# Performance work log

Measured on AMD Instinct MI355X. Metric: run time of the kernel, lower is better.

Reference implementation:

```python
import jax, jax.numpy as jnp
import numpy as np

B, N, D, K = 2, 8192, 512, 16


def setup_inputs() -> dict:
    key = jax.random.key(0)
    k1, k2, k3, k4 = jax.random.split(key, 4)
    x = jax.random.normal(k1, (B, N, D), dtype=jnp.float32)
    xyz = jax.random.normal(k2, (B, N, 3), dtype=jnp.float32)
    # nn.Linear(d_model, 3*d_model): weight [3D, D], bias [3D]
    W_qkv = jax.random.normal(k3, (3 * D, D), dtype=jnp.float32) * 0.02
    b_qkv = jnp.zeros((3 * D,), dtype=jnp.float32)
    # nn.Linear(d_model, d_model)
    W_fc = jax.random.normal(k4, (D, D), dtype=jnp.float32) * 0.02
    b_fc = jnp.zeros((D,), dtype=jnp.float32)
    return {"x": x, "xyz": xyz, "W_qkv": W_qkv, "b_qkv": b_qkv, "W_fc": W_fc, "b_fc": b_fc}


def _knn_idx(xyz):
    # squared-distance KNN (same ordering as cdist): |a|^2 + |b|^2 - 2 a.b
    sq = jnp.sum(xyz * xyz, axis=-1)                      # [B, N]
    d2 = sq[:, :, None] + sq[:, None, :] - 2.0 * jnp.einsum('bnc,bmc->bnm', xyz, xyz)
    return jax.lax.top_k(-d2, K)[1]                       # [B, N, K] smallest distances


def reference(x, xyz, W_qkv, b_qkv, W_fc, b_fc):
    knn_idx = _knn_idx(xyz)                               # no-grad in original
    qkv = jnp.einsum('bnd,ed->bne', x, W_qkv) + b_qkv     # [B, N, 3D]
    qkv = qkv.reshape(B, N, 3, D)
    q, k, v = qkv[:, :, 0], qkv[:, :, 1], qkv[:, :, 2]    # [B, N, D]
    gather = jax.vmap(lambda arr, idx: arr[idx])          # per-batch neighbor gather
    k_neigh = gather(k, knn_idx)                          # [B, N, K, D]
    v_neigh = gather(v, knn_idx)                          # [B, N, K, D]
    # faithful to einsum('bnd,bnsk->bns', q, k_neigh): sums d and feature dims independently
    attn = (q.sum(-1)[:, :, None] * k_neigh.sum(-1)) / jnp.sqrt(jnp.float32(D))  # [B, N, K]
    attn = jax.nn.softmax(attn, axis=2)[..., None]        # [B, N, K, 1]
    x_out = (attn * v_neigh).sum(axis=2)                  # [B, N, D]
    return jnp.einsum('bnd,ed->bne', x_out, W_fc) + b_fc + x
```

## Files before the change

### kernel.cpp

```cpp
#include <hip/hip_runtime.h>

typedef _Float16 half_t;
typedef _Float16 half8 __attribute__((ext_vector_type(8)));
typedef _Float16 half4v __attribute__((ext_vector_type(4)));
typedef float f32x4 __attribute__((ext_vector_type(4)));
typedef float f32x2 __attribute__((ext_vector_type(2)));

#define NB 2
#define NN 8192
#define ND 512
#define NKNN 16
#define BN (NB*NN)

#define OFF_XH   0ull
#define OFF_VH   (OFF_XH  + (size_t)BN*ND*2)
#define OFF_XOH  (OFF_VH  + (size_t)BN*ND*2)
#define OFF_WVH  (OFF_XOH + (size_t)BN*ND*2)
#define OFF_WFCH (OFF_WVH + (size_t)ND*ND*2)
#define OFF_XW   (OFF_WFCH+ (size_t)ND*ND*2)
#define OFF_XW2  (OFF_XW  + (size_t)BN*16)
#define OFF_IDX  (OFF_XW2 + (size_t)BN*16)
#define OFF_WQC  (OFF_IDX + (size_t)BN*NKNN*4)
#define OFF_WKC  (OFF_WQC + 2048)
#define OFF_QKB  (OFF_WKC + 2048)
#define OFF_QS   (OFF_QKB + 256)
#define OFF_KS   (OFF_QS  + (size_t)BN*4)

__global__ __launch_bounds__(256) void kcolsum(const float* __restrict__ W,
                                               float* __restrict__ wq,
                                               float* __restrict__ wk) {
  int h = blockIdx.x >> 3, g = blockIdx.x & 7;
  int t = threadIdx.x, dl = t & 63, s = t >> 6;
  const float* Wb = W + (size_t)h * 512 * 512;
  int d = g * 64 + dl;
  float acc = 0.f;
  for (int e = s * 128; e < s * 128 + 128; ++e) acc += Wb[(size_t)e * 512 + d];
  __shared__ float red[4][64];
  red[s][dl] = acc;
  __syncthreads();
  if (s == 0) (h ? wk : wq)[d] = red[0][dl] + red[1][dl] + red[2][dl] + red[3][dl];
}

__global__ __launch_bounds__(512) void kbias(const float* __restrict__ b,
                                             float* __restrict__ qkb) {
  __shared__ float r0[512], r1[512];
  int t = threadIdx.x;
  r0[t] = b[t]; r1[t] = b[512 + t];
  __syncthreads();
  for (int s = 256; s; s >>= 1) {
    if (t < s) { r0[t] += r0[t + s]; r1[t] += r1[t + s]; }
    __syncthreads();
  }
  if (t == 0) { qkb[0] = r0[0]; qkb[1] = r1[0]; }
}

__global__ __launch_bounds__(256) void kconvw(const float* __restrict__ wqkv,
                                              const float* __restrict__ wfc,
                                              half_t* __restrict__ wvh,
                                              half_t* __restrict__ wfch) {
  int i = blockIdx.x * 256 + threadIdx.x;
  float4 a = ((const float4*)(wqkv + 1024 * 512))[i];
  half4v ha; ha[0]=(half_t)a.x; ha[1]=(half_t)a.y; ha[2]=(half_t)a.z; ha[3]=(half_t)a.w;
  *(half4v*)(wvh + (size_t)i * 4) = ha;
  float4 c = ((const float4*)wfc)[i];
  half4v hc; hc[0]=(half_t)c.x; hc[1]=(half_t)c.y; hc[2]=(half_t)c.z; hc[3]=(half_t)c.w;
  *(half4v*)(wfch + (size_t)i * 4) = hc;
}

__global__ __launch_bounds__(256) void kxh(const float* __restrict__ x,
                                           const float* __restrict__ wq,
                                           const float* __restrict__ wk,
                                           const float* __restrict__ qkb,
                                           half_t* __restrict__ xh,
                                           float* __restrict__ qs,
                                           float* __restrict__ ks) {
  int wid = blockIdx.x * 4 + (threadIdx.x >> 6);
  int l = threadIdx.x & 63;
  size_t base = (size_t)wid * ND + l * 8;
  float4 a0 = *(const float4*)(x + base);
  float4 a1 = *(const float4*)(x + base + 4);
  half8 h;
  h[0]=(half_t)a0.x; h[1]=(half_t)a0.y; h[2]=(half_t)a0.z; h[3]=(half_t)a0.w;
  h[4]=(half_t)a1.x; h[5]=(half_t)a1.y; h[6]=(half_t)a1.z; h[7]=(half_t)a1.w;
  *(half8*)(xh + base) = h;
  float4 q0 = ((const float4*)(wq + l * 8))[0], q1 = ((const float4*)(wq + l * 8))[1];
  float4 k0 = ((const float4*)(wk + l * 8))[0], k1 = ((const float4*)(wk + l * 8))[1];
  float dq = a0.x*q0.x + a0.y*q0.y + a0.z*q0.z + a0.w*q0.w
           + a1.x*q1.x + a1.y*q1.y + a1.z*q1.z + a1.w*q1.w;
  float dk = a0.x*k0.x + a0.y*k0.y + a0.z*k0.z + a0.w*k0.w
           + a1.x*k1.x + a1.y*k1.y + a1.z*k1.z + a1.w*k1.w;
  #pragma unroll
  for (int o = 32; o; o >>= 1) { dq += __shfl_xor(dq, o); dk += __shfl_xor(dk, o); }
  if (l == 0) { qs[wid] = dq + qkb[0]; ks[wid] = dk + qkb[1]; }
}

__global__ __launch_bounds__(256) void kxyzw(const float* __restrict__ xyz,
                                             float4* __restrict__ xw,
                                             float4* __restrict__ xw2) {
  int p = blockIdx.x * 256 + threadIdx.x;
  int b = p >> 12;
  int pl = p & 4095;
  int i0 = b * NN + pl * 2;
  const float* s = xyz + (size_t)i0 * 3;
  float x0 = s[0], y0 = s[1], z0 = s[2];
  float x1 = s[3], y1 = s[4], z1 = s[5];
  float sq0 = __fadd_rn(__fadd_rn(__fmul_rn(x0, x0), __fmul_rn(y0, y0)), __fmul_rn(z0, z0));
  float sq1 = __fadd_rn(__fadd_rn(__fmul_rn(x1, x1), __fmul_rn(y1, y1)), __fmul_rn(z1, z1));
  xw[i0]     = make_float4(x0, y0, z0, sq0);
  xw[i0 + 1] = make_float4(x1, y1, z1, sq1);
  xw2[(size_t)b * NN + pl]          = make_float4(x0, x1, y0, y1);
  xw2[(size_t)b * NN + NN/2 + pl]   = make_float4(z0, z1, sq0, sq1);
}

#define QPW 4
__global__ __launch_bounds__(256, 4) void kknn(const float4* __restrict__ xw,
                                               const float4* __restrict__ xw2,
                                               int* __restrict__ idxo) {
  const int tid = threadIdx.x;
  const int l = tid & 63;
  const int b = blockIdx.x >> 9;
  const int qbase = (blockIdx.x & 511) * (4 * QPW) + (tid >> 6) * QPW;
  const float4* xb  = xw  + (size_t)b * NN;
  const float4* xa2 = xw2 + (size_t)b * NN;
  const float4* xb2 = xa2 + NN / 2;

  f32x2 qxx[QPW], qyy[QPW], qzz[QPW], qww[QPW];
  #pragma unroll
  for (int qi = 0; qi < QPW; ++qi) {
    float4 qp = xb[qbase + qi];
    qxx[qi] = (f32x2){qp.x, qp.x};
    qyy[qi] = (f32x2){qp.y, qp.y};
    qzz[qi] = (f32x2){qp.z, qp.z};
    qww[qi] = (f32x2){qp.w, qp.w};
  }
  const f32x2 m2 = (f32x2){-2.0f, -2.0f};

  float mind0[QPW], mind1[QPW]; int mini0[QPW], mini1[QPW];
  #pragma unroll
  for (int qi = 0; qi < QPW; ++qi) {
    mind0[qi] = __builtin_inff(); mini0[qi] = 0x7fffffff;
    mind1[qi] = __builtin_inff(); mini1[qi] = 0x7fffffff;
  }

  auto body1 = [&](const float4& A, const float4& Bv, int it) {
    f32x2 cx = (f32x2){A.x, A.y};
    f32x2 cy = (f32x2){A.z, A.w};
    f32x2 cz = (f32x2){Bv.x, Bv.y};
    f32x2 cw = (f32x2){Bv.z, Bv.w};
    int ci0 = (it * 64 + l) * 2;
    #pragma unroll
    for (int qi = 0; qi < QPW; ++qi) {
      f32x2 dot = __builtin_elementwise_fma(qzz[qi], cz,
                    __builtin_elementwise_fma(qyy[qi], cy, qxx[qi] * cx));
      f32x2 s2 = qww[qi] + cw;
      f32x2 d2 = __builtin_elementwise_fma(m2, dot, s2);
      if (d2.x < mind0[qi]) { mind0[qi] = d2.x; mini0[qi] = ci0; }
      if (d2.y < mind1[qi]) { mind1[qi] = d2.y; mini1[qi] = ci0 + 1; }
    }
  };

  {
    float4 A0 = xa2[l],      B0 = xb2[l];
    float4 A1 = xa2[64 + l], B1 = xb2[64 + l];
    for (int tt = 0; tt < 4; ++tt) {
      __syncthreads();
      #pragma unroll
      for (int its = 0; its < 16; its += 2) {
        int it = tt * 16 + its;
        int pf = it + 2; if (pf > 62) pf = 62;
        float4 A2 = xa2[pf * 64 + l];
        float4 B2 = xb2[pf * 64 + l];
        float4 A3 = xa2[pf * 64 + 64 + l];
        float4 B3 = xb2[pf * 64 + 64 + l];
        body1(A0, B0, it);
        body1(A1, B1, it + 1);
        A0 = A2; B0 = B2; A1 = A3; B1 = B3;
      }
    }
  }

  float mind[QPW]; int mini[QPW];
  #pragma unroll
  for (int qi = 0; qi < QPW; ++qi) {
    bool take1 = (mind1[qi] < mind0[qi]) ||
                 (mind1[qi] == mind0[qi] && mini1[qi] < mini0[qi]);
    mind[qi] = take1 ? mind1[qi] : mind0[qi];
    mini[qi] = take1 ? mini1[qi] : mini0[qi];
  }

  float kd[QPW]; int ki[QPW]; float wst[QPW];
  #pragma unroll
  for (int qi = 0; qi < QPW; ++qi) {
    float d = mind[qi]; int ii = mini[qi];
    #pragma unroll
    for (int k = 2; k <= 64; k <<= 1) {
      #pragma unroll
      for (int j = k >> 1; j > 0; j >>= 1) {
        float od = __shfl_xor(d, j);
        int   oi = __shfl_xor(ii, j);
        bool up = ((l & k) == 0);
        bool lower_lane = ((l & j) == 0);
        bool oless = (od < d) || (od == d && oi < ii);
        bool take = (up == lower_lane) ? oless : !oless;
        if (take) { d = od; ii = oi; }
      }
    }
    kd[qi] = __shfl(d, l & 15);
    ki[qi] = __shfl(ii, l & 15);
    wst[qi] = __shfl(d, 15);
  }

  auto insert = [&](bool ok, float dv, int iv, int qi) {
    unsigned long long m = __ballot(ok);
    while (m) {
      int a = __builtin_ctzll(m);
      m &= m - 1;
      float dc = __shfl(dv, a);
      int ic = __shfl(iv, a);
      bool lower = (kd[qi] < dc) || (kd[qi] == dc && ki[qi] < ic);
      int r = __popcll(__ballot(lower) & 0xFFFFull);
      if (r < 16) {
        float pd = __shfl_up(kd[qi], 1, 16);
        int pi = __shfl_up(ki[qi], 1, 16);
        int pp = l & 15;
        if (pp == r)      { kd[qi] = dc; ki[qi] = ic; }
        else if (pp > r)  { kd[qi] = pd; ki[qi] = pi; }
        wst[qi] = __shfl(kd[qi], 15, 16);
      }
    }
  };

  auto body2 = [&](const float4& A, const float4& Bv, int it) {
    f32x2 cx = (f32x2){A.x, A.y};
    f32x2 cy = (f32x2){A.z, A.w};
    f32x2 cz = (f32x2){Bv.x, Bv.y};
    f32x2 cw = (f32x2){Bv.z, Bv.w};
    int ci0 = (it * 64 + l) * 2;
    #pragma unroll
    for (int qi = 0; qi < QPW; ++qi) {
      f32x2 dot = __builtin_elementwise_fma(qzz[qi], cz,
                    __builtin_elementwise_fma(qyy[qi], cy, qxx[qi] * cx));
      f32x2 s2 = qww[qi] + cw;
      f32x2 d2 = __builtin_elementwise_fma(m2, dot, s2);
      bool ok0 = (d2.x <= wst[qi]) && (ci0 != mini[qi]);
      bool ok1 = (d2.y <= wst[qi]) && (ci0 + 1 != mini[qi]);
      insert(ok0, d2.x, ci0, qi);
      insert(ok1, d2.y, ci0 + 1, qi);
    }
  };

  {
    float4 A0 = xa2[l],      B0 = xb2[l];
    float4 A1 = xa2[64 + l], B1 = xb2[64 + l];
    for (int tt = 0; tt < 4; ++tt) {
      __syncthreads();
      #pragma unroll
      for (int its = 0; its < 16; its += 2) {
        int it = tt * 16 + its;
        int pf = it + 2; if (pf > 62) pf = 62;
        float4 A2 = xa2[pf * 64 + l];
        float4 B2 = xb2[pf * 64 + l];
        float4 A3 = xa2[pf * 64 + 64 + l];
        float4 B3 = xb2[pf * 64 + 64 + l];
        body2(A0, B0, it);
        body2(A1, B1, it + 1);
        A0 = A2; B0 = B2; A1 = A3; B1 = B3;
      }
    }
  }

  if (l < 16) {
    #pragma unroll
    for (int qi = 0; qi < QPW; ++qi)
      idxo[((size_t)b * NN + qbase + qi) * NKNN + l] = ki[qi];
  }
}

__device__ __forceinline__ void gload16(const void* g, void* l) {
  __builtin_amdgcn_global_load_lds((const __attribute__((address_space(1))) void*)g,
                                   (__attribute__((address_space(3))) void*)l, 16, 0, 0);
}

template <int EPI>
__global__ __launch_bounds__(256) void kgemm(const half_t* __restrict__ A,
                                             const half_t* __restrict__ Bw,
                                             const float* __restrict__ bias,
                                             const float* __restrict__ resid,
                                             void* __restrict__ Cout) {
  __shared__ __align__(16) half_t As[128 * 64];
  __shared__ __align__(16) half_t Bs[128 * 64];
  const int tid = threadIdx.x;
  const int l = tid & 63;
  const int w = tid >> 6;
  const int wm = w >> 1, wn = w & 1;
  const int mt = blockIdx.x >> 2;
  const int nt = blockIdx.x & 3;
  const int lr = l & 15, lg = l >> 4;

  f32x4 acc[4][4];
  #pragma unroll
  for (int i = 0; i < 4; ++i)
    #pragma unroll
    for (int j = 0; j < 4; ++j) acc[i][j] = (f32x4){0.f, 0.f, 0.f, 0.f};

  for (int kt = 0; kt < 8; ++kt) {
    #pragma unroll
    for (int i = 0; i < 4; ++i) {
      int id = i * 256 + tid;
      int rr = id >> 3, cc = id & 7;
      gload16(A + (size_t)(mt * 128 + rr) * ND + kt * 64 + cc * 8,
              (void*)(As + (size_t)(i * 256 + w * 64) * 8));
      gload16(Bw + (size_t)(nt * 128 + rr) * ND + kt * 64 + cc * 8,
              (void*)(Bs + (size_t)(i * 256 + w * 64) * 8));
    }
    __syncthreads();
    #pragma unroll
    for (int kk = 0; kk < 2; ++kk) {
      half8 af[4], bf[4];
      #pragma unroll
      for (int mi = 0; mi < 4; ++mi)
        af[mi] = *(const half8*)(As + (wm * 64 + mi * 16 + lr) * 64 + kk * 32 + lg * 8);
      #pragma unroll
      for (int ni = 0; ni < 4; ++ni)
        bf[ni] = *(const half8*)(Bs + (wn * 64 + ni * 16 + lr) * 64 + kk * 32 + lg * 8);
      #pragma unroll
      for (int mi = 0; mi < 4; ++mi)
        #pragma unroll
        for (int ni = 0; ni < 4; ++ni)
          acc[mi][ni] = __builtin_amdgcn_mfma_f32_16x16x32_f16(af[mi], bf[ni], acc[mi][ni], 0, 0, 0);
    }
    __syncthreads();
  }

  #pragma unroll
  for (int mi = 0; mi < 4; ++mi) {
    #pragma unroll
    for (int ni = 0; ni < 4; ++ni) {
      int col = nt * 128 + wn * 64 + ni * 16 + lr;
      #pragma unroll
      for (int r4 = 0; r4 < 4; ++r4) {
        size_t row = (size_t)mt * 128 + wm * 64 + mi * 16 + lg * 4 + r4;
        float v = acc[mi][ni][r4] + bias[col];
        if (EPI == 0) ((half_t*)Cout)[row * ND + col] = (half_t)v;
        else          ((float*)Cout)[row * ND + col] = v + resid[row * ND + col];
      }
    }
  }
}

__global__ __launch_bounds__(256) void kattn(const int* __restrict__ idx,
                                             const float* __restrict__ qs,
                                             const float* __restrict__ ks,
                                             const half_t* __restrict__ vh,
                                             half_t* __restrict__ xoh) {
  int wid = blockIdx.x * 4 + (threadIdx.x >> 6);
  int l = threadIdx.x & 63;
  int b = wid >> 13;
  int j = l & 15;
  int nb = idx[(size_t)wid * NKNN + j];
  float ksv = ks[(size_t)b * NN + nb];
  float logit = __fdiv_rn(__fmul_rn(qs[wid], ksv), 22.627416997969522f);
  float mx = logit;
  #pragma unroll
  for (int o = 8; o; o >>= 1) mx = fmaxf(mx, __shfl_xor(mx, o, 16));
  float e = expf(logit - mx);
  float s = e;
  #pragma unroll
  for (int o = 8; o; o >>= 1) s += __shfl_xor(s, o, 16);
  float p = e / s;

  float acc[8] = {0.f, 0.f, 0.f, 0.f, 0.f, 0.f, 0.f, 0.f};
  #pragma unroll
  for (int t16 = 0; t16 < 16; ++t16) {
    float wj = __shfl(p, t16, 16);
    int ij = __shfl(nb, t16, 16);
    const half8 vv = *(const half8*)(vh + ((size_t)b * NN + ij) * ND + l * 8);
    #pragma unroll
    for (int u = 0; u < 8; ++u) acc[u] += wj * (float)vv[u];
  }
  half8 ho;
  #pragma unroll
  for (int u = 0; u < 8; ++u) ho[u] = (half_t)acc[u];
  *(half8*)(xoh + (size_t)wid * ND + l * 8) = ho;
}

extern "C" void kernel_launch(void* const* d_in, const int* in_sizes, int n_in,
                              void* d_out, int out_size, void* d_ws, size_t ws_size,
                              hipStream_t stream) {
  const float* x    = (const float*)d_in[0];
  const float* xyz  = (const float*)d_in[1];
  const float* wqkv = (const float*)d_in[2];
  const float* bqkv = (const float*)d_in[3];
  const float* wfc  = (const float*)d_in[4];
  const float* bfc  = (const float*)d_in[5];
  char* ws = (char*)d_ws;
  half_t* xh   = (half_t*)(ws + OFF_XH);
  half_t* vh   = (half_t*)(ws + OFF_VH);
  half_t* xoh  = (half_t*)(ws + OFF_XOH);
  half_t* wvh  = (half_t*)(ws + OFF_WVH);
  half_t* wfch = (half_t*)(ws + OFF_WFCH);
  float4* xw   = (float4*)(ws + OFF_XW);
  float4* xw2  = (float4*)(ws + OFF_XW2);
  int*    idx  = (int*)(ws + OFF_IDX);
  float*  wqc  = (float*)(ws + OFF_WQC);
  float*  wkc  = (float*)(ws + OFF_WKC);
  float*  qkb  = (float*)(ws + OFF_QKB);
  float*  qs   = (float*)(ws + OFF_QS);
  float*  ks   = (float*)(ws + OFF_KS);

  kcolsum<<<dim3(16),  dim3(256), 0, stream>>>(wqkv, wqc, wkc);
  kbias  <<<dim3(1),   dim3(512), 0, stream>>>(bqkv, qkb);
  kconvw <<<dim3(256), dim3(256), 0, stream>>>(wqkv, wfc, wvh, wfch);
  kxyzw  <<<dim3(32),  dim3(256), 0, stream>>>(xyz, xw, xw2);
  kxh    <<<dim3(4096),dim3(256), 0, stream>>>(x, wqc, wkc, qkb, xh, qs, ks);
  kknn   <<<dim3(1024),dim3(256), 0, stream>>>(xw, xw2, idx);
  kgemm<0><<<dim3(512),dim3(256), 0, stream>>>(xh, wvh, bqkv + 1024, (const float*)nullptr, (void*)vh);
  kattn  <<<dim3(4096),dim3(256), 0, stream>>>(idx, qs, ks, vh, xoh);
  kgemm<1><<<dim3(512),dim3(256), 0, stream>>>(xoh, wfch, bfc, x, d_out);
}
```

Baseline: 167.2 us.

## Merge setup kernels and co-schedule KNN, q/k sums and V GEMM in one launch

Four small setup kernels are folded into one block-indexed launch. KNN, the q/k row-sum computation and the V projection GEMM now run as role-partitioned blocks of a single grid, so their independent work can overlap on the GPU. The fp16 copy of x is dropped: the GEMM blocks read fp32 x and convert it to half in registers before writing LDS, which removes one global round trip. The risk is that the heterogeneous blocks compete for occupancy, since the KNN launch bound now also applies to the GEMM blocks. The GEMM's A-side load also changes from the asynchronous global-to-LDS path to synchronous register loads.

```diff
diff --git a/kernel.cpp b/kernel.cpp
--- a/kernel.cpp
+++ b/kernel.cpp
@@ -26,323 +26,322 @@
 #define OFF_QS   (OFF_QKB + 256)
 #define OFF_KS   (OFF_QS  + (size_t)BN*4)
 
-__global__ __launch_bounds__(256) void kcolsum(const float* __restrict__ W,
-                                               float* __restrict__ wq,
-                                               float* __restrict__ wk) {
-  int h = blockIdx.x >> 3, g = blockIdx.x & 7;
-  int t = threadIdx.x, dl = t & 63, s = t >> 6;
-  const float* Wb = W + (size_t)h * 512 * 512;
-  int d = g * 64 + dl;
-  float acc = 0.f;
-  for (int e = s * 128; e < s * 128 + 128; ++e) acc += Wb[(size_t)e * 512 + d];
-  __shared__ float red[4][64];
-  red[s][dl] = acc;
-  __syncthreads();
-  if (s == 0) (h ? wk : wq)[d] = red[0][dl] + red[1][dl] + red[2][dl] + red[3][dl];
-}
-
-__global__ __launch_bounds__(512) void kbias(const float* __restrict__ b,
-                                             float* __restrict__ qkb) {
-  __shared__ float r0[512], r1[512];
-  int t = threadIdx.x;
-  r0[t] = b[t]; r1[t] = b[512 + t];
-  __syncthreads();
-  for (int s = 256; s; s >>= 1) {
-    if (t < s) { r0[t] += r0[t + s]; r1[t] += r1[t + s]; }
-    __syncthreads();
-  }
-  if (t == 0) { qkb[0] = r0[0]; qkb[1] = r1[0]; }
-}
-
-__global__ __launch_bounds__(256) void kconvw(const float* __restrict__ wqkv,
-                                              const float* __restrict__ wfc,
-                                              half_t* __restrict__ wvh,
-                                              half_t* __restrict__ wfch) {
-  int i = blockIdx.x * 256 + threadIdx.x;
-  float4 a = ((const float4*)(wqkv + 1024 * 512))[i];
-  half4v ha; ha[0]=(half_t)a.x; ha[1]=(half_t)a.y; ha[2]=(half_t)a.z; ha[3]=(half_t)a.w;
-  *(half4v*)(wvh + (size_t)i * 4) = ha;
-  float4 c = ((const float4*)wfc)[i];
-  half4v hc; hc[0]=(half_t)c.x; hc[1]=(half_t)c.y; hc[2]=(half_t)c.z; hc[3]=(half_t)c.w;
-  *(half4v*)(wfch + (size_t)i * 4) = hc;
-}
-
-__global__ __launch_bounds__(256) void kxh(const float* __restrict__ x,
-                                           const float* __restrict__ wq,
-                                           const float* __restrict__ wk,
-                                           const float* __restrict__ qkb,
-                                           half_t* __restrict__ xh,
-                                           float* __restrict__ qs,
-                                           float* __restrict__ ks) {
-  int wid = blockIdx.x * 4 + (threadIdx.x >> 6);
-  int l = threadIdx.x & 63;
-  size_t base = (size_t)wid * ND + l * 8;
-  float4 a0 = *(const float4*)(x + base);
-  float4 a1 = *(const float4*)(x + base + 4);
-  half8 h;
-  h[0]=(half_t)a0.x; h[1]=(half_t)a0.y; h[2]=(half_t)a0.z; h[3]=(half_t)a0.w;
-  h[4]=(half_t)a1.x; h[5]=(half_t)a1.y; h[6]=(half_t)a1.z; h[7]=(half_t)a1.w;
-  *(half8*)(xh + base) = h;
-  float4 q0 = ((const float4*)(wq + l * 8))[0], q1 = ((const float4*)(wq + l * 8))[1];
-  float4 k0 = ((const float4*)(wk + l * 8))[0], k1 = ((const float4*)(wk + l * 8))[1];
-  float dq = a0.x*q0.x + a0.y*q0.y + a0.z*q0.z + a0.w*q0.w
-           + a1.x*q1.x + a1.y*q1.y + a1.z*q1.z + a1.w*q1.w;
-  float dk = a0.x*k0.x + a0.y*k0.y + a0.z*k0.z + a0.w*k0.w
-           + a1.x*k1.x + a1.y*k1.y + a1.z*k1.z + a1.w*k1.w;
-  #pragma unroll
-  for (int o = 32; o; o >>= 1) { dq += __shfl_xor(dq, o); dk += __shfl_xor(dk, o); }
-  if (l == 0) { qs[wid] = dq + qkb[0]; ks[wid] = dk + qkb[1]; }
-}
-
-__global__ __launch_bounds__(256) void kxyzw(const float* __restrict__ xyz,
-                                             float4* __restrict__ xw,
-                                             float4* __restrict__ xw2) {
-  int p = blockIdx.x * 256 + threadIdx.x;
-  int b = p >> 12;
-  int pl = p & 4095;
-  int i0 = b * NN + pl * 2;
-  const float* s = xyz + (size_t)i0 * 3;
-  float x0 = s[0], y0 = s[1], z0 = s[2];
-  float x1 = s[3], y1 = s[4], z1 = s[5];
-  float sq0 = __fadd_rn(__fadd_rn(__fmul_rn(x0, x0), __fmul_rn(y0, y0)), __fmul_rn(z0, z0));
-  float sq1 = __fadd_rn(__fadd_rn(__fmul_rn(x1, x1), __fmul_rn(y1, y1)), __fmul_rn(z1, z1));
-  xw[i0]     = make_float4(x0, y0, z0, sq0);
-  xw[i0 + 1] = make_float4(x1, y1, z1, sq1);
-  xw2[(size_t)b * NN + pl]          = make_float4(x0, x1, y0, y1);
-  xw2[(size_t)b * NN + NN/2 + pl]   = make_float4(z0, z1, sq0, sq1);
-}
-
-#define QPW 4
-__global__ __launch_bounds__(256, 4) void kknn(const float4* __restrict__ xw,
-                                               const float4* __restrict__ xw2,
-                                               int* __restrict__ idxo) {
-  const int tid = threadIdx.x;
-  const int l = tid & 63;
-  const int b = blockIdx.x >> 9;
-  const int qbase = (blockIdx.x & 511) * (4 * QPW) + (tid >> 6) * QPW;
-  const float4* xb  = xw  + (size_t)b * NN;
-  const float4* xa2 = xw2 + (size_t)b * NN;
-  const float4* xb2 = xa2 + NN / 2;
-
-  f32x2 qxx[QPW], qyy[QPW], qzz[QPW], qww[QPW];
-  #pragma unroll
-  for (int qi = 0; qi < QPW; ++qi) {
-    float4 qp = xb[qbase + qi];
-    qxx[qi] = (f32x2){qp.x, qp.x};
-    qyy[qi] = (f32x2){qp.y, qp.y};
-    qzz[qi] = (f32x2){qp.z, qp.z};
-    qww[qi] = (f32x2){qp.w, qp.w};
-  }
-  const f32x2 m2 = (f32x2){-2.0f, -2.0f};
-
-  float mind0[QPW], mind1[QPW]; int mini0[QPW], mini1[QPW];
-  #pragma unroll
-  for (int qi = 0; qi < QPW; ++qi) {
-    mind0[qi] = __builtin_inff(); mini0[qi] = 0x7fffffff;
-    mind1[qi] = __builtin_inff(); mini1[qi] = 0x7fffffff;
-  }
-
-  auto body1 = [&](const float4& A, const float4& Bv, int it) {
-    f32x2 cx = (f32x2){A.x, A.y};
-    f32x2 cy = (f32x2){A.z, A.w};
-    f32x2 cz = (f32x2){Bv.x, Bv.y};
-    f32x2 cw = (f32x2){Bv.z, Bv.w};
-    int ci0 = (it * 64 + l) * 2;
-    #pragma unroll
-    for (int qi = 0; qi < QPW; ++qi) {
-      f32x2 dot = __builtin_elementwise_fma(qzz[qi], cz,
-                    __builtin_elementwise_fma(qyy[qi], cy, qxx[qi] * cx));
-      f32x2 s2 = qww[qi] + cw;
-      f32x2 d2 = __builtin_elementwise_fma(m2, dot, s2);
-      if (d2.x < mind0[qi]) { mind0[qi] = d2.x; mini0[qi] = ci0; }
-      if (d2.y < mind1[qi]) { mind1[qi] = d2.y; mini1[qi] = ci0 + 1; }
-    }
-  };
-
-  {
-    float4 A0 = xa2[l],      B0 = xb2[l];
-    float4 A1 = xa2[64 + l], B1 = xb2[64 + l];
-    for (int tt = 0; tt < 4; ++tt) {
-      __syncthreads();
-      #pragma unroll
-      for (int its = 0; its < 16; its += 2) {
-        int it = tt * 16 + its;
-        int pf = it + 2; if (pf > 62) pf = 62;
-        float4 A2 = xa2[pf * 64 + l];
-        float4 B2 = xb2[pf * 64 + l];
-        float4 A3 = xa2[pf * 64 + 64 + l];
-        float4 B3 = xb2[pf * 64 + 64 + l];
-        body1(A0, B0, it);
-        body1(A1, B1, it + 1);
-        A0 = A2; B0 = B2; A1 = A3; B1 = B3;
-      }
-    }
-  }
-
-  float mind[QPW]; int mini[QPW];
-  #pragma unroll
-  for (int qi = 0; qi < QPW; ++qi) {
-    bool take1 = (mind1[qi] < mind0[qi]) ||
-                 (mind1[qi] == mind0[qi] && mini1[qi] < mini0[qi]);
-    mind[qi] = take1 ? mind1[qi] : mind0[qi];
-    mini[qi] = take1 ? mini1[qi] : mini0[qi];
-  }
-
-  float kd[QPW]; int ki[QPW]; float wst[QPW];
-  #pragma unroll
-  for (int qi = 0; qi < QPW; ++qi) {
-    float d = mind[qi]; int ii = mini[qi];
-    #pragma unroll
-    for (int k = 2; k <= 64; k <<= 1) {
-      #pragma unroll
-      for (int j = k >> 1; j > 0; j >>= 1) {
-        float od = __shfl_xor(d, j);
-        int   oi = __shfl_xor(ii, j);
-        bool up = ((l & k) == 0);
-        bool lower_lane = ((l & j) == 0);
-        bool oless = (od < d) || (od == d && oi < ii);
-        bool take = (up == lower_lane) ? oless : !oless;
-        if (take) { d = od; ii = oi; }
-      }
-    }
-    kd[qi] = __shfl(d, l & 15);
-    ki[qi] = __shfl(ii, l & 15);
-    wst[qi] = __shfl(d, 15);
-  }
-
-  auto insert = [&](bool ok, float dv, int iv, int qi) {
-    unsigned long long m = __ballot(ok);
-    while (m) {
-      int a = __builtin_ctzll(m);
-      m &= m - 1;
-      float dc = __shfl(dv, a);
-      int ic = __shfl(iv, a);
-      bool lower = (kd[qi] < dc) || (kd[qi] == dc && ki[qi] < ic);
-      int r = __popcll(__ballot(lower) & 0xFFFFull);
-      if (r < 16) {
-        float pd = __shfl_up(kd[qi], 1, 16);
-        int pi = __shfl_up(ki[qi], 1, 16);
-        int pp = l & 15;
-        if (pp == r)      { kd[qi] = dc; ki[qi] = ic; }
-        else if (pp > r)  { kd[qi] = pd; ki[qi] = pi; }
-        wst[qi] = __shfl(kd[qi], 15, 16);
-      }
-    }
-  };
-
-  auto body2 = [&](const float4& A, const float4& Bv, int it) {
-    f32x2 cx = (f32x2){A.x, A.y};
-    f32x2 cy = (f32x2){A.z, A.w};
-    f32x2 cz = (f32x2){Bv.x, Bv.y};
-    f32x2 cw = (f32x2){Bv.z, Bv.w};
-    int ci0 = (it * 64 + l) * 2;
-    #pragma unroll
-    for (int qi = 0; qi < QPW; ++qi) {
-      f32x2 dot = __builtin_elementwise_fma(qzz[qi], cz,
-                    __builtin_elementwise_fma(qyy[qi], cy, qxx[qi] * cx));
-      f32x2 s2 = qww[qi] + cw;
-      f32x2 d2 = __builtin_elementwise_fma(m2, dot, s2);
-      bool ok0 = (d2.x <= wst[qi]) && (ci0 != mini[qi]);
-      bool ok1 = (d2.y <= wst[qi]) && (ci0 + 1 != mini[qi]);
-      insert(ok0, d2.x, ci0, qi);
-      insert(ok1, d2.y, ci0 + 1, qi);
-    }
-  };
-
-  {
-    float4 A0 = xa2[l],      B0 = xb2[l];
-    float4 A1 = xa2[64 + l], B1 = xb2[64 + l];
-    for (int tt = 0; tt < 4; ++tt) {
-      __syncthreads();
-      #pragma unroll
-      for (int its = 0; its < 16; its += 2) {
-        int it = tt * 16 + its;
-        int pf = it + 2; if (pf > 62) pf = 62;
-        float4 A2 = xa2[pf * 64 + l];
-        float4 B2 = xb2[pf * 64 + l];
-        float4 A3 = xa2[pf * 64 + 64 + l];
-        float4 B3 = xb2[pf * 64 + 64 + l];
-        body2(A0, B0, it);
-        body2(A1, B1, it + 1);
-        A0 = A2; B0 = B2; A1 = A3; B1 = B3;
-      }
-    }
-  }
-
-  if (l < 16) {
-    #pragma unroll
-    for (int qi = 0; qi < QPW; ++qi)
-      idxo[((size_t)b * NN + qbase + qi) * NKNN + l] = ki[qi];
-  }
-}
-
 __device__ __forceinline__ void gload16(const void* g, void* l) {
   __builtin_amdgcn_global_load_lds((const __attribute__((address_space(1))) void*)g,
                                    (__attribute__((address_space(3))) void*)l, 16, 0, 0);
 }
 
-template <int EPI>
-__global__ __launch_bounds__(256) void kgemm(const half_t* __restrict__ A,
-                                             const half_t* __restrict__ Bw,
-                                             const float* __restrict__ bias,
-                                             const float* __restrict__ resid,
-                                             void* __restrict__ Cout) {
-  __shared__ __align__(16) half_t As[128 * 64];
-  __shared__ __align__(16) half_t Bs[128 * 64];
+__global__ __launch_bounds__(256) void ksetup(const float* __restrict__ wqkv,
+                                              const float* __restrict__ bqkv,
+                                              const float* __restrict__ wfc,
+                                              const float* __restrict__ xyz,
+                                              float* __restrict__ wq, float* __restrict__ wk,
+                                              float* __restrict__ qkb,
+                                              half_t* __restrict__ wvh, half_t* __restrict__ wfch,
+                                              float4* __restrict__ xw, float4* __restrict__ xw2) {
+  const int blk = blockIdx.x;
+  const int t = threadIdx.x;
+  if (blk < 16) {
+    int h = blk >> 3, g = blk & 7;
+    int dl = t & 63, s = t >> 6;
+    const float* Wb = wqkv + (size_t)h * 512 * 512;
+    int d = g * 64 + dl;
+    float acc = 0.f;
+    for (int e = s * 128; e < s * 128 + 128; ++e) acc += Wb[(size_t)e * 512 + d];
+    __shared__ float red[4][64];
+    red[s][dl] = acc;
+    __syncthreads();
+    if (s == 0) (h ? wk : wq)[d] = red[0][dl] + red[1][dl] + red[2][dl] + red[3][dl];
+  } else if (blk == 16) {
+    __shared__ float r0[256], r1[256];
+    r0[t] = bqkv[t] + bqkv[t + 256];
+    r1[t] = bqkv[512 + t] + bqkv[768 + t];
+    __syncthreads();
+    for (int s = 128; s; s >>= 1) {
+      if (t < s) { r0[t] += r0[t + s]; r1[t] += r1[t + s]; }
+      __syncthreads();
+    }
+    if (t == 0) { qkb[0] = r0[0]; qkb[1] = r1[0]; }
+  } else if (blk < 273) {
+    int i = (blk - 17) * 256 + t;
+    float4 a = ((const float4*)(wqkv + 1024 * 512))[i];
+    half4v ha; ha[0]=(half_t)a.x; ha[1]=(half_t)a.y; ha[2]=(half_t)a.z; ha[3]=(half_t)a.w;
+    *(half4v*)(wvh + (size_t)i * 4) = ha;
+    float4 c = ((const float4*)wfc)[i];
+    half4v hc; hc[0]=(half_t)c.x; hc[1]=(half_t)c.y; hc[2]=(half_t)c.z; hc[3]=(half_t)c.w;
+    *(half4v*)(wfch + (size_t)i * 4) = hc;
+  } else {
+    int p = (blk - 273) * 256 + t;
+    int b = p >> 12;
+    int pl = p & 4095;
+    int i0 = b * NN + pl * 2;
+    const float* s = xyz + (size_t)i0 * 3;
+    float x0 = s[0], y0 = s[1], z0 = s[2];
+    float x1 = s[3], y1 = s[4], z1 = s[5];
+    float sq0 = __fadd_rn(__fadd_rn(__fmul_rn(x0, x0), __fmul_rn(y0, y0)), __fmul_rn(z0, z0));
+    float sq1 = __fadd_rn(__fadd_rn(__fmul_rn(x1, x1), __fmul_rn(y1, y1)), __fmul_rn(z1, z1));
+    xw[i0]     = make_float4(x0, y0, z0, sq0);
+    xw[i0 + 1] = make_float4(x1, y1, z1, sq1);
+    xw2[(size_t)b * NN + pl]        = make_float4(x0, x1, y0, y1);
+    xw2[(size_t)b * NN + NN/2 + pl] = make_float4(z0, z1, sq0, sq1);
+  }
+}
+
+#define QPW 4
+__global__ __launch_bounds__(256, 4) void kbig(const float4* __restrict__ xw,
+                                               const float4* __restrict__ xw2,
+                                               int* __restrict__ idxo,
+                                               const float* __restrict__ x,
+                                               const float* __restrict__ wq,
+                                               const float* __restrict__ wk,
+                                               const float* __restrict__ qkb,
+                                               float* __restrict__ qs,
+                                               float* __restrict__ ks,
+                                               const half_t* __restrict__ wvh,
+                                               const float* __restrict__ bv,
+                                               half_t* __restrict__ vh) {
+  const int g5 = blockIdx.x / 5;
+  const int r5 = blockIdx.x % 5;
   const int tid = threadIdx.x;
   const int l = tid & 63;
   const int w = tid >> 6;
-  const int wm = w >> 1, wn = w & 1;
-  const int mt = blockIdx.x >> 2;
-  const int nt = blockIdx.x & 3;
-  const int lr = l & 15, lg = l >> 4;
-
-  f32x4 acc[4][4];
-  #pragma unroll
-  for (int i = 0; i < 4; ++i)
-    #pragma unroll
-    for (int j = 0; j < 4; ++j) acc[i][j] = (f32x4){0.f, 0.f, 0.f, 0.f};
-
-  for (int kt = 0; kt < 8; ++kt) {
-    #pragma unroll
-    for (int i = 0; i < 4; ++i) {
-      int id = i * 256 + tid;
-      int rr = id >> 3, cc = id & 7;
-      gload16(A + (size_t)(mt * 128 + rr) * ND + kt * 64 + cc * 8,
-              (void*)(As + (size_t)(i * 256 + w * 64) * 8));
-      gload16(Bw + (size_t)(nt * 128 + rr) * ND + kt * 64 + cc * 8,
-              (void*)(Bs + (size_t)(i * 256 + w * 64) * 8));
-    }
-    __syncthreads();
-    #pragma unroll
-    for (int kk = 0; kk < 2; ++kk) {
-      half8 af[4], bf[4];
-      #pragma unroll
-      for (int mi = 0; mi < 4; ++mi)
-        af[mi] = *(const half8*)(As + (wm * 64 + mi * 16 + lr) * 64 + kk * 32 + lg * 8);
-      #pragma unroll
-      for (int ni = 0; ni < 4; ++ni)
-        bf[ni] = *(const half8*)(Bs + (wn * 64 + ni * 16 + lr) * 64 + kk * 32 + lg * 8);
-      #pragma unroll
-      for (int mi = 0; mi < 4; ++mi)
+
+  if (r5 < 2) {
+    const int bid = g5 * 2 + r5;
+    const int b = bid >> 9;
+    const int qbase = (bid & 511) * (4 * QPW) + w * QPW;
+    const float4* xb  = xw  + (size_t)b * NN;
+    const float4* xa2 = xw2 + (size_t)b * NN;
+    const float4* xb2 = xa2 + NN / 2;
+
+    f32x2 qxx[QPW], qyy[QPW], qzz[QPW], qww[QPW];
+    #pragma unroll
+    for (int qi = 0; qi < QPW; ++qi) {
+      float4 qp = xb[qbase + qi];
+      qxx[qi] = (f32x2){qp.x, qp.x};
+      qyy[qi] = (f32x2){qp.y, qp.y};
+      qzz[qi] = (f32x2){qp.z, qp.z};
+      qww[qi] = (f32x2){qp.w, qp.w};
+    }
+    const f32x2 m2 = (f32x2){-2.0f, -2.0f};
+
+    float mind0[QPW], mind1[QPW]; int mini0[QPW], mini1[QPW];
+    #pragma unroll
+    for (int qi = 0; qi < QPW; ++qi) {
+      mind0[qi] = __builtin_inff(); mini0[qi] = 0x7fffffff;
+      mind1[qi] = __builtin_inff(); mini1[qi] = 0x7fffffff;
+    }
+
+    auto body1 = [&](const float4& A, const float4& Bv, int it) {
+      f32x2 cx = (f32x2){A.x, A.y};
+      f32x2 cy = (f32x2){A.z, A.w};
+      f32x2 cz = (f32x2){Bv.x, Bv.y};
+      f32x2 cw = (f32x2){Bv.z, Bv.w};
+      int ci0 = (it * 64 + l) * 2;
+      #pragma unroll
+      for (int qi = 0; qi < QPW; ++qi) {
+        f32x2 dot = __builtin_elementwise_fma(qzz[qi], cz,
+                      __builtin_elementwise_fma(qyy[qi], cy, qxx[qi] * cx));
+        f32x2 s2 = qww[qi] + cw;
+        f32x2 d2 = __builtin_elementwise_fma(m2, dot, s2);
+        if (d2.x < mind0[qi]) { mind0[qi] = d2.x; mini0[qi] = ci0; }
+        if (d2.y < mind1[qi]) { mind1[qi] = d2.y; mini1[qi] = ci0 + 1; }
+      }
+    };
+
+    {
+      float4 A0 = xa2[l],      B0 = xb2[l];
+      float4 A1 = xa2[64 + l], B1 = xb2[64 + l];
+      for (int tt = 0; tt < 4; ++tt) {
+        __syncthreads();
+        #pragma unroll
+        for (int its = 0; its < 16; its += 2) {
+          int it = tt * 16 + its;
+          int pf = it + 2; if (pf > 62) pf = 62;
+          float4 A2 = xa2[pf * 64 + l];
+          float4 B2 = xb2[pf * 64 + l];
+          float4 A3 = xa2[pf * 64 + 64 + l];
+          float4 B3 = xb2[pf * 64 + 64 + l];
+          body1(A0, B0, it);
+          body1(A1, B1, it + 1);
+          A0 = A2; B0 = B2; A1 = A3; B1 = B3;
+        }
+      }
+    }
+
+    float mind[QPW]; int mini[QPW];
+    #pragma unroll
+    for (int qi = 0; qi < QPW; ++qi) {
+      bool take1 = (mind1[qi] < mind0[qi]) ||
+                   (mind1[qi] == mind0[qi] && mini1[qi] < mini0[qi]);
+      mind[qi] = take1 ? mind1[qi] : mind0[qi];
+      mini[qi] = take1 ? mini1[qi] : mini0[qi];
+    }
+
+    float kd[QPW]; int ki[QPW]; float wst[QPW];
+    #pragma unroll
+    for (int qi = 0; qi < QPW; ++qi) {
+      float d = mind[qi]; int ii = mini[qi];
+      #pragma unroll
+      for (int k = 2; k <= 64; k <<= 1) {
+        #pragma unroll
+        for (int j = k >> 1; j > 0; j >>= 1) {
+          float od = __shfl_xor(d, j);
+          int   oi = __shfl_xor(ii, j);
+          bool up = ((l & k) == 0);
+          bool lower_lane = ((l & j) == 0);
+          bool oless = (od < d) || (od == d && oi < ii);
+          bool take = (up == lower_lane) ? oless : !oless;
+          if (take) { d = od; ii = oi; }
+        }
+      }
+      kd[qi] = __shfl(d, l & 15);
+      ki[qi] = __shfl(ii, l & 15);
+      wst[qi] = __shfl(d, 15);
+    }
+
+    auto insert = [&](bool ok, float dv, int iv, int qi) {
+      unsigned long long m = __ballot(ok);
+      while (m) {
+        int a = __builtin_ctzll(m);
+        m &= m - 1;
+        float dc = __shfl(dv, a);
+        int ic = __shfl(iv, a);
+        bool lower = (kd[qi] < dc) || (kd[qi] == dc && ki[qi] < ic);
+        int r = __popcll(__ballot(lower) & 0xFFFFull);
+        if (r < 16) {
+          float pd = __shfl_up(kd[qi], 1, 16);
+          int pi = __shfl_up(ki[qi], 1, 16);
+          int pp = l & 15;
+          if (pp == r)      { kd[qi] = dc; ki[qi] = ic; }
+          else if (pp > r)  { kd[qi] = pd; ki[qi] = pi; }
+          wst[qi] = __shfl(kd[qi], 15, 16);
+        }
+      }
+    };
+
+    auto body2 = [&](const float4& A, const float4& Bv, int it) {
+      f32x2 cx = (f32x2){A.x, A.y};
+      f32x2 cy = (f32x2){A.z, A.w};
+      f32x2 cz = (f32x2){Bv.x, Bv.y};
+      f32x2 cw = (f32x2){Bv.z, Bv.w};
+      int ci0 = (it * 64 + l) * 2;
+      #pragma unroll
+      for (int qi = 0; qi < QPW; ++qi) {
+        f32x2 dot = __builtin_elementwise_fma(qzz[qi], cz,
+                      __builtin_elementwise_fma(qyy[qi], cy, qxx[qi] * cx));
+        f32x2 s2 = qww[qi] + cw;
+        f32x2 d2 = __builtin_elementwise_fma(m2, dot, s2);
+        bool ok0 = (d2.x <= wst[qi]) && (ci0 != mini[qi]);
+        bool ok1 = (d2.y <= wst[qi]) && (ci0 + 1 != mini[qi]);
+        insert(ok0, d2.x, ci0, qi);
+        insert(ok1, d2.y, ci0 + 1, qi);
+      }
+    };
+
+    {
+      float4 A0 = xa2[l],      B0 = xb2[l];
+      float4 A1 = xa2[64 + l], B1 = xb2[64 + l];
+      for (int tt = 0; tt < 4; ++tt) {
+        __syncthreads();
+        #pragma unroll
+        for (int its = 0; its < 16; its += 2) {
+          int it = tt * 16 + its;
+          int pf = it + 2; if (pf > 62) pf = 62;
+          float4 A2 = xa2[pf * 64 + l];
+          float4 B2 = xb2[pf * 64 + l];
+          float4 A3 = xa2[pf * 64 + 64 + l];
+          float4 B3 = xb2[pf * 64 + 64 + l];
+          body2(A0, B0, it);
+          body2(A1, B1, it + 1);
+          A0 = A2; B0 = B2; A1 = A3; B1 = B3;
+        }
+      }
+    }
+
+    if (l < 16) {
+      #pragma unroll
+      for (int qi = 0; qi < QPW; ++qi)
+        idxo[((size_t)b * NN + qbase + qi) * NKNN + l] = ki[qi];
+    }
+  } else if (r5 < 4) {
+    const int bid = g5 * 2 + (r5 - 2);
+    float4 q0 = ((const float4*)(wq + l * 8))[0], q1 = ((const float4*)(wq + l * 8))[1];
+    float4 k0 = ((const float4*)(wk + l * 8))[0], k1 = ((const float4*)(wk + l * 8))[1];
+    float qb0 = qkb[0], qb1 = qkb[1];
+    #pragma unroll
+    for (int rr = 0; rr < 4; ++rr) {
+      int wid = bid * 16 + w * 4 + rr;
+      size_t base = (size_t)wid * ND + l * 8;
+      float4 a0 = *(const float4*)(x + base);
+      float4 a1 = *(const float4*)(x + base + 4);
+      float dq = a0.x*q0.x + a0.y*q0.y + a0.z*q0.z + a0.w*q0.w
+               + a1.x*q1.x + a1.y*q1.y + a1.z*q1.z + a1.w*q1.w;
+      float dk = a0.x*k0.x + a0.y*k0.y + a0.z*k0.z + a0.w*k0.w
+               + a1.x*k1.x + a1.y*k1.y + a1.z*k1.z + a1.w*k1.w;
+      #pragma unroll
+      for (int o = 32; o; o >>= 1) { dq += __shfl_xor(dq, o); dk += __shfl_xor(dk, o); }
+      if (l == 0) { qs[wid] = dq + qb0; ks[wid] = dk + qb1; }
+    }
+  } else {
+    __shared__ __align__(16) half_t As[128 * 64];
+    __shared__ __align__(16) half_t Bs[128 * 64];
+    const int gbid = g5;
+    const int wm = w >> 1, wn = w & 1;
+    const int mt = gbid >> 2;
+    const int nt = gbid & 3;
+    const int lr = l & 15, lg = l >> 4;
+
+    f32x4 acc[4][4];
+    #pragma unroll
+    for (int i = 0; i < 4; ++i)
+      #pragma unroll
+      for (int j = 0; j < 4; ++j) acc[i][j] = (f32x4){0.f, 0.f, 0.f, 0.f};
+
+    for (int kt = 0; kt < 8; ++kt) {
+      #pragma unroll
+      for (int i = 0; i < 4; ++i) {
+        int id = i * 256 + tid;
+        int rr = id >> 3, cc = id & 7;
+        const float* src = x + (size_t)(mt * 128 + rr) * ND + kt * 64 + cc * 8;
+        float4 f0 = *(const float4*)src;
+        float4 f1 = *(const float4*)(src + 4);
+        half8 h;
+        h[0]=(half_t)f0.x; h[1]=(half_t)f0.y; h[2]=(half_t)f0.z; h[3]=(half_t)f0.w;
+        h[4]=(half_t)f1.x; h[5]=(half_t)f1.y; h[6]=(half_t)f1.z; h[7]=(half_t)f1.w;
+        *(half8*)(As + (size_t)id * 8) = h;
+        gload16(wvh + (size_t)(nt * 128 + rr) * ND + kt * 64 + cc * 8,
+                (void*)(Bs + (size_t)(i * 256 + w * 64) * 8));
+      }
+      __syncthreads();
+      #pragma unroll
+      for (int kk = 0; kk < 2; ++kk) {
+        half8 af[4], bf[4];
+        #pragma unroll
+        for (int mi = 0; mi < 4; ++mi)
+          af[mi] = *(const half8*)(As + (wm * 64 + mi * 16 + lr) * 64 + kk * 32 + lg * 8);
         #pragma unroll
         for (int ni = 0; ni < 4; ++ni)
-          acc[mi][ni] = __builtin_amdgcn_mfma_f32_16x16x32_f16(af[mi], bf[ni], acc[mi][ni], 0, 0, 0);
-    }
-    __syncthreads();
-  }
-
-  #pragma unroll
-  for (int mi = 0; mi < 4; ++mi) {
-    #pragma unroll
-    for (int ni = 0; ni < 4; ++ni) {
-      int col = nt * 128 + wn * 64 + ni * 16 + lr;
-      #pragma unroll
-      for (int r4 = 0; r4 < 4; ++r4) {
-        size_t row = (size_t)mt * 128 + wm * 64 + mi * 16 + lg * 4 + r4;
-        float v = acc[mi][ni][r4] + bias[col];
-        if (EPI == 0) ((half_t*)Cout)[row * ND + col] = (half_t)v;
-        else          ((float*)Cout)[row * ND + col] = v + resid[row * ND + col];
+          bf[ni] = *(const half8*)(Bs + (wn * 64 + ni * 16 + lr) * 64 + kk * 32 + lg * 8);
+        #pragma unroll
+        for (int mi = 0; mi < 4; ++mi)
+          #pragma unroll
+          for (int ni = 0; ni < 4; ++ni)
+            acc[mi][ni] = __builtin_amdgcn_mfma_f32_16x16x32_f16(af[mi], bf[ni], acc[mi][ni], 0, 0, 0);
+      }
+      __syncthreads();
+    }
+
+    #pragma unroll
+    for (int mi = 0; mi < 4; ++mi) {
+      #pragma unroll
+      for (int ni = 0; ni < 4; ++ni) {
+        int col = nt * 128 + wn * 64 + ni * 16 + lr;
+        #pragma unroll
+        for (int r4 = 0; r4 < 4; ++r4) {
+          size_t row = (size_t)mt * 128 + wm * 64 + mi * 16 + lg * 4 + r4;
+          vh[row * ND + col] = (half_t)(acc[mi][ni][r4] + bv[col]);
+        }
       }
     }
   }
@@ -384,6 +383,70 @@
   *(half8*)(xoh + (size_t)wid * ND + l * 8) = ho;
 }
 
+__global__ __launch_bounds__(256) void kgemm1(const half_t* __restrict__ A,
+                                              const half_t* __restrict__ Bw,
+                                              const float* __restrict__ bias,
+                                              const float* __restrict__ resid,
+                                              float* __restrict__ Cout) {
+  __shared__ __align__(16) half_t As[128 * 64];
+  __shared__ __align__(16) half_t Bs[128 * 64];
+  const int tid = threadIdx.x;
+  const int l = tid & 63;
+  const int w = tid >> 6;
+  const int wm = w >> 1, wn = w & 1;
+  const int mt = blockIdx.x >> 2;
+  const int nt = blockIdx.x & 3;
+  const int lr = l & 15, lg = l >> 4;
+
+  f32x4 acc[4][4];
+  #pragma unroll
+  for (int i = 0; i < 4; ++i)
+    #pragma unroll
+    for (int j = 0; j < 4; ++j) acc[i][j] = (f32x4){0.f, 0.f, 0.f, 0.f};
+
+  for (int kt = 0; kt < 8; ++kt) {
+    #pragma unroll
+    for (int i = 0; i < 4; ++i) {
+      int id = i * 256 + tid;
+      int rr = id >> 3, cc = id & 7;
+      gload16(A + (size_t)(mt * 128 + rr) * ND + kt * 64 + cc * 8,
+              (void*)(As + (size_t)(i * 256 + w * 64) * 8));
+      gload16(Bw + (size_t)(nt * 128 + rr) * ND + kt * 64 + cc * 8,
+              (void*)(Bs + (size_t)(i * 256 + w * 64) * 8));
+    }
+    __syncthreads();
+    #pragma unroll
+    for (int kk = 0; kk < 2; ++kk) {
+      half8 af[4], bf[4];
+      #pragma unroll
+      for (int mi = 0; mi < 4; ++mi)
+        af[mi] = *(const half8*)(As + (wm * 64 + mi * 16 + lr) * 64 + kk * 32 + lg * 8);
+      #pragma unroll
+      for (int ni = 0; ni < 4; ++ni)
+        bf[ni] = *(const half8*)(Bs + (wn * 64 + ni * 16 + lr) * 64 + kk * 32 + lg * 8);
+      #pragma unroll
+      for (int mi = 0; mi < 4; ++mi)
+        #pragma unroll
+        for (int ni = 0; ni < 4; ++ni)
+          acc[mi][ni] = __builtin_amdgcn_mfma_f32_16x16x32_f16(af[mi], bf[ni], acc[mi][ni], 0, 0, 0);
+    }
+    __syncthreads();
+  }
+
+  #pragma unroll
+  for (int mi = 0; mi < 4; ++mi) {
+    #pragma unroll
+    for (int ni = 0; ni < 4; ++ni) {
+      int col = nt * 128 + wn * 64 + ni * 16 + lr;
+      #pragma unroll
+      for (int r4 = 0; r4 < 4; ++r4) {
+        size_t row = (size_t)mt * 128 + wm * 64 + mi * 16 + lg * 4 + r4;
+        Cout[row * ND + col] = acc[mi][ni][r4] + bias[col] + resid[row * ND + col];
+      }
+    }
+  }
+}
+
 extern "C" void kernel_launch(void* const* d_in, const int* in_sizes, int n_in,
                               void* d_out, int out_size, void* d_ws, size_t ws_size,
                               hipStream_t stream) {
@@ -394,7 +457,6 @@
   const float* wfc  = (const float*)d_in[4];
   const float* bfc  = (const float*)d_in[5];
   char* ws = (char*)d_ws;
-  half_t* xh   = (half_t*)(ws + OFF_XH);
   half_t* vh   = (half_t*)(ws + OFF_VH);
   half_t* xoh  = (half_t*)(ws + OFF_XOH);
   half_t* wvh  = (half_t*)(ws + OFF_WVH);
@@ -408,13 +470,10 @@
   float*  qs   = (float*)(ws + OFF_QS);
   float*  ks   = (float*)(ws + OFF_KS);
 
-  kcolsum<<<dim3(16),  dim3(256), 0, stream>>>(wqkv, wqc, wkc);
-  kbias  <<<dim3(1),   dim3(512), 0, stream>>>(bqkv, qkb);
-  kconvw <<<dim3(256), dim3(256), 0, stream>>>(wqkv, wfc, wvh, wfch);
-  kxyzw  <<<dim3(32),  dim3(256), 0, stream>>>(xyz, xw, xw2);
-  kxh    <<<dim3(4096),dim3(256), 0, stream>>>(x, wqc, wkc, qkb, xh, qs, ks);
-  kknn   <<<dim3(1024),dim3(256), 0, stream>>>(xw, xw2, idx);
-  kgemm<0><<<dim3(512),dim3(256), 0, stream>>>(xh, wvh, bqkv + 1024, (const float*)nullptr, (void*)vh);
-  kattn  <<<dim3(4096),dim3(256), 0, stream>>>(idx, qs, ks, vh, xoh);
-  kgemm<1><<<dim3(512),dim3(256), 0, stream>>>(xoh, wfch, bfc, x, d_out);
-}
+  ksetup<<<dim3(305), dim3(256), 0, stream>>>(wqkv, bqkv, wfc, xyz,
+                                              wqc, wkc, qkb, wvh, wfch, xw, xw2);
+  kbig  <<<dim3(2560),dim3(256), 0, stream>>>(xw, xw2, idx, x, wqc, wkc, qkb,
+                                              qs, ks, wvh, bqkv + 1024, vh);
+  kattn <<<dim3(4096),dim3(256), 0, stream>>>(idx, qs, ks, vh, xoh);
+  kgemm1<<<dim3(512), dim3(256), 0, stream>>>(xoh, wfch, bfc, x, (float*)d_out);
+}
```

Measured after the change: 172.3 us. 3.1% more time.
